# Kernel optimization log

Hardware: AMD Instinct MI355X
Metric: run time of the kernel (lower is better)

The kernel has to match this reference:

```python
import jax, jax.numpy as jnp
import numpy as np

WAY, NQ, C, H = 5, 150, 640, 10
TEMP, TEMP_ATTN = 0.2, 5.0


def _conv2d(x, w):
    return jax.lax.conv_general_dilated(x, w, (1, 1), ((0, 0), (0, 0)),
                                        dimension_numbers=('NCHW', 'OIHW', 'NCHW'))


def _conv3d(x, w, pad):
    return jax.lax.conv_general_dilated(x, w, (1, 1, 1), pad,
                                        dimension_numbers=('NCDHW', 'OIDHW', 'NCDHW'))


def _affine(x, g, b):
    # eval-mode BatchNorm folded to per-channel affine
    sh = (1, -1) + (1,) * (x.ndim - 2)
    return x * g.reshape(sh) + b.reshape(sh)


def _gnorm(x, axis, eps=1e-5):
    m = jnp.mean(x, axis=axis, keepdims=True)
    v = jnp.var(x, axis=axis, ddof=1, keepdims=True)  # torch.var is unbiased
    return (x - m) / jnp.sqrt(v + eps)


def _sep_conv4d(x, w2, g2, b2, w1, g1, b1, wp, gp, bp):
    # RENet SepConv4d: 3x3 conv over (Hs,Ws), relu, 3x3 conv over (Hq,Wq), 1x1 channel proj
    B, c, u, v, h, w = x.shape
    y = x.reshape(B, c, u, v, h * w)
    y = _conv3d(y, w2, ((1, 1), (1, 1), (0, 0)))  # kernel (3,3,1) over (u,v)
    y = jax.nn.relu(_affine(y, g2, b2))
    y = y.reshape(B, c, u * v, h, w)
    y = _conv3d(y, w1, ((0, 0), (1, 1), (1, 1)))  # kernel (1,3,3) over (h,w)
    y = _affine(y, g1, b1)
    y = _conv2d(y.reshape(B, c, u * v * h, w), wp)  # 1x1 projection to out channels
    y = _affine(y, gp, bp)
    return y.reshape(B, wp.shape[0], u, v, h, w)


def setup_inputs() -> dict:
    key = jax.random.key(0)
    ks = jax.random.split(key, 10)
    d = {}
    d['spt'] = jax.random.normal(ks[0], (1, WAY, C, H, H), jnp.float32)
    d['qry'] = jax.random.normal(ks[1], (NQ, C, H, H), jnp.float32)
    d['cca1x1_w'] = jax.random.normal(ks[2], (64, C, 1, 1), jnp.float32) * 0.05
    d['cca1x1_g'] = jnp.ones((64,), jnp.float32)
    d['cca1x1_b'] = jnp.zeros((64,), jnp.float32)
    # SepConv4d layer 0: 1 -> 16 channels
    d['s0_w2'] = jax.random.normal(ks[3], (1, 1, 3, 3, 1), jnp.float32) * 0.3
    d['s0_g2'] = jnp.ones((1,), jnp.float32); d['s0_b2'] = jnp.zeros((1,), jnp.float32)
    d['s0_w1'] = jax.random.normal(ks[4], (1, 1, 1, 3, 3), jnp.float32) * 0.3
    d['s0_g1'] = jnp.ones((1,), jnp.float32); d['s0_b1'] = jnp.zeros((1,), jnp.float32)
    d['s0_wp'] = jax.random.normal(ks[5], (16, 1, 1, 1), jnp.float32) * 0.3
    d['s0_gp'] = jnp.ones((16,), jnp.float32); d['s0_bp'] = jnp.zeros((16,), jnp.float32)
    # SepConv4d layer 1: 16 -> 1 channels
    d['s1_w2'] = jax.random.normal(ks[6], (16, 16, 3, 3, 1), jnp.float32) * 0.1
    d['s1_g2'] = jnp.ones((16,), jnp.float32); d['s1_b2'] = jnp.zeros((16,), jnp.float32)
    d['s1_w1'] = jax.random.normal(ks[7], (16, 16, 1, 3, 3), jnp.float32) * 0.1
    d['s1_g1'] = jnp.ones((16,), jnp.float32); d['s1_b1'] = jnp.zeros((16,), jnp.float32)
    d['s1_wp'] = jax.random.normal(ks[8], (1, 16, 1, 1), jnp.float32) * 0.3
    d['s1_gp'] = jnp.ones((1,), jnp.float32); d['s1_bp'] = jnp.zeros((1,), jnp.float32)
    return d


def reference(spt, qry, cca1x1_w, cca1x1_g, cca1x1_b,
              s0_w2, s0_g2, s0_b2, s0_w1, s0_g1, s0_b1, s0_wp, s0_gp, s0_bp,
              s1_w2, s1_g2, s1_b2, s1_w1, s1_g1, s1_b1, s1_wp, s1_gp, s1_bp):
    spt = spt[0]                                             # [way, C, H, W]
    spt = spt - jnp.mean(spt, axis=1, keepdims=True)         # normalize_feature
    qry = qry - jnp.mean(qry, axis=1, keepdims=True)

    def feat(x):
        y = jax.nn.relu(_affine(_conv2d(x, cca1x1_w), cca1x1_g, cca1x1_b))
        n = jnp.sqrt(jnp.sum(y * y, axis=1, keepdims=True))
        return y / jnp.maximum(n, 1e-8)                      # F.normalize(p=2, dim=1)

    s, q = feat(spt), feat(qry)                              # [way,64,H,W], [nq,64,H,W]
    corr = jnp.einsum('wcij,qckl->qwijkl', s, q)             # [nq,way,Hs,Ws,Hq,Wq]
    nq, way, Hs, Ws, Hq, Wq = corr.shape

    x = corr.reshape(nq * way, 1, Hs, Ws, Hq, Wq)
    x = _sep_conv4d(x, s0_w2, s0_g2, s0_b2, s0_w1, s0_g1, s0_b1, s0_wp, s0_gp, s0_bp)
    x = jax.nn.relu(x)
    x = _sep_conv4d(x, s1_w2, s1_g2, s1_b2, s1_w1, s1_g1, s1_b1, s1_wp, s1_gp, s1_bp)

    cs = _gnorm(x.reshape(nq, way, Hs * Ws, Hq, Wq), 2)
    cq = _gnorm(x.reshape(nq, way, Hs, Ws, Hq * Wq), 4)
    a_s = jax.nn.softmax(cs / TEMP_ATTN, axis=2).reshape(nq, way, Hs, Ws, Hq, Wq).sum(axis=(4, 5))
    a_q = jax.nn.softmax(cq / TEMP_ATTN, axis=4).reshape(nq, way, Hs, Ws, Hq, Wq).sum(axis=(2, 3))

    sp = (a_s[:, :, None] * spt[None]).mean(axis=(-1, -2))   # [nq,way,C]
    qp = (a_q[:, :, None] * qry[:, None]).mean(axis=(-1, -2))
    num = jnp.sum(sp * qp, axis=-1)
    den = jnp.maximum(jnp.linalg.norm(sp, axis=-1), 1e-8) * jnp.maximum(jnp.linalg.norm(qp, axis=-1), 1e-8)
    return (num / den) / TEMP                                # [nq, way]
```

## Files before the change

kernel.cpp:

```cpp
#include <hip/hip_runtime.h>
#include <cstdint>
#include <cstddef>

#define NQT   150
#define WAYT  5
#define CCH   640

typedef _Float16 f16;
typedef _Float16 f16x2 __attribute__((ext_vector_type(2)));
typedef _Float16 f16x4 __attribute__((ext_vector_type(4)));
typedef _Float16 f16x8 __attribute__((ext_vector_type(8)));
typedef float    f32x4 __attribute__((ext_vector_type(4)));

static __device__ __forceinline__ f16x2 pkrtz(float a, float b){
  return __builtin_bit_cast(f16x2, __builtin_amdgcn_cvt_pkrtz(a, b));
}

#define CP_A     0
#define CP_B     16
#define CP_G2    32
#define CP_B2    48
#define CP_W20   64
#define CP_W10   73
#define CP_SC    82
#define CP_T9    96
#define GS_STRIDE 1076

static __device__ __forceinline__ float stencil9(int k, int n, const float* __restrict__ w9){
  if (k >= 100 || n >= 100) return 0.f;
  const int a = n/10, b = n%10, a2 = k/10, b2 = k%10;
  const int dA = a2 - a + 1, dB = b2 - b + 1;
  if ((unsigned)dA > 2u || (unsigned)dB > 2u) return 0.f;
  return w9[dA*3 + dB];
}

__global__ __launch_bounds__(256) void k_prep_all(
    const float* __restrict__ W,
    const float* __restrict__ s0_w2, const float* __restrict__ s0_g2, const float* __restrict__ s0_b2,
    const float* __restrict__ s0_w1, const float* __restrict__ s0_g1, const float* __restrict__ s0_b1,
    const float* __restrict__ s0_wp, const float* __restrict__ s0_gp, const float* __restrict__ s0_bp,
    const float* __restrict__ s1_w2, const float* __restrict__ s1_g2, const float* __restrict__ s1_b2,
    const float* __restrict__ s1_w1, const float* __restrict__ s1_g1, const float* __restrict__ s1_b1,
    const float* __restrict__ s1_wp, const float* __restrict__ s1_gp, const float* __restrict__ s1_bp,
    float* __restrict__ cp, f16* __restrict__ Apack, f16* __restrict__ Wf2,
    f16* __restrict__ MuF, f16* __restrict__ MhF,
    f16* __restrict__ W65, float* __restrict__ wsum)
{
  const int b = blockIdx.x, t = threadIdx.x;
  if (b == 0){
    for (int e = t; e < 2560; e += 256){
      int p = e / 512, r = e % 512, l = r / 8, j = r % 8;
      int kb = l >> 4;
      int tap = 2*p + (kb >> 1);
      int cin = (kb & 1)*8 + j;
      int co = l & 15;
      float v = 0.f;
      if (tap <= 8){
        int du = tap / 3, dv = tap % 3;
        v = s1_w2[((co*16 + cin)*3 + du)*3 + dv];
      }
      Apack[e] = (f16)v;
    }
    const float gp1 = s1_gp[0];
    {
      int l = t >> 2, j = t & 3;
      int tap = l & 15, ci = ((l >> 4) << 2) + j;
      float v = 0.f;
      if (tap <= 8){
        for (int co = 0; co < 16; co++)
          v += gp1 * s1_wp[co] * s1_g1[co] * s1_w1[(co*16 + ci)*9 + tap];
      }
      Wf2[t] = (f16)v;
    }
    if (t < 144){
      int tap = t / 16, co = t % 16;
      float s = 0.f;
      for (int cin = 0; cin < 16; cin++){
        float wv = (float)(f16)s1_w2[((co*16 + cin)*3 + tap/3)*3 + tap%3];
        float rb = fmaxf((float)(f16)s0_bp[cin], 0.f);
        s += wv * rb;
      }
      cp[CP_T9 + t] = s;
    }
    if (t < 16){
      cp[CP_A + t]  = s0_gp[t] * s0_wp[t];
      cp[CP_B + t]  = s0_bp[t];
      cp[CP_G2 + t] = s1_g2[t];
      cp[CP_B2 + t] = s1_b2[t];
    }
    if (t < 9){ cp[CP_W20 + t] = s0_w2[t]; cp[CP_W10 + t] = s0_w1[t]; }
    if (t == 0){
      cp[CP_SC + 0] = s0_g2[0]; cp[CP_SC + 1] = s0_b2[0];
      cp[CP_SC + 2] = s0_g1[0]; cp[CP_SC + 3] = s0_b1[0];
      float kk = 0.f;
      for (int co = 0; co < 16; co++) kk += s1_wp[co] * s1_b1[co];
      cp[CP_SC + 4] = gp1 * kk + s1_bp[0];
    }
  } else if (b <= 14){
    const bool isMu = (b <= 7);
    f16* dst = isMu ? MuF : MhF;
    const float* w9 = isMu ? s0_w2 : s0_w1;
    const int base = (isMu ? (b-1) : (b-8)) * 2048;
    #pragma unroll
    for (int e2 = 0; e2 < 8; e2++){
      const int idx = base + e2*256 + t;
      const int j = idx & 7, l2 = (idx >> 3) & 63, ktnt = idx >> 9;
      const int kt = ktnt & 3, nt = ktnt >> 2;
      const int n = nt*16 + (l2 & 15);
      const int k = kt*32 + ((l2 >> 4) & 3)*8 + j;
      dst[idx] = (f16)stencil9(k, n, w9);
    }
  } else if (b <= 39){
    const int base = (b - 15) * 2048;
    #pragma unroll
    for (int e2 = 0; e2 < 8; e2++){
      const int idx = base + e2*256 + t;
      const int row = idx / 640, c = idx - row*640;
      float v = 0.f;
      if (row < 64) v = W[row*640 + c];
      else if (row == 64) v = 1.f;
      W65[idx] = (f16)v;
    }
  } else {
    const int o = t >> 2, qq = t & 3;
    float s = 0.f;
    for (int c = qq; c < 640; c += 4) s += W[o*640 + c];
    s += __shfl_xor(s, 1); s += __shfl_xor(s, 2);
    if (qq == 0) wsum[o] = s;
  }
}

__device__ __forceinline__ void feat_stage(const float* __restrict__ x, int kt, f16* __restrict__ dst, int t){
  for (int e = t; e < 800; e += 256){
    const int cc = e & 31, qd = e >> 5;
    const float4 v4 = ((const float4*)(x + (size_t)(kt*32 + cc)*100))[qd];
    const int pb = qd*4;
    dst[(pb+0)*40 + cc] = (f16)v4.x;
    dst[(pb+1)*40 + cc] = (f16)v4.y;
    dst[(pb+2)*40 + cc] = (f16)v4.z;
    dst[(pb+3)*40 + cc] = (f16)v4.w;
  }
}

__global__ __launch_bounds__(256) void k_feat(
    const float* __restrict__ spt, const float* __restrict__ qry,
    const f16* __restrict__ W65, const float* __restrict__ wsum,
    const float* __restrict__ gg, const float* __restrict__ bb,
    f16* __restrict__ s16, f16* __restrict__ q16,
    float* __restrict__ sptm, float* __restrict__ qrym)
{
  __shared__ f16 Xs[2][112*40];
  __shared__ float Ys[112*85];
  __shared__ float sg[64], sb[64], sw[64];
  const int n = blockIdx.x;
  const float* x; f16* out16; float* mout;
  if (n < 5){ x = spt + (size_t)n*64000; out16 = s16 + (size_t)n*7168; mout = sptm + n*100; }
  else { x = qry + (size_t)(n-5)*64000; out16 = q16 + (size_t)(n-5)*7168; mout = qrym + (size_t)(n-5)*100; }
  const int t = threadIdx.x, l = t & 63, wid = t >> 6;
  const int r16 = l & 15, kbq = (l >> 4) & 3;

  int mts[9], nts[9];
  #pragma unroll
  for (int s = 0; s < 9; s++){ const int mn = wid + s*4; mts[s] = mn/7; nts[s] = mn - (mn/7)*7; }
  f32x4 acc[9];
  #pragma unroll
  for (int s = 0; s < 9; s++) acc[s] = (f32x4){0.f,0.f,0.f,0.f};

  feat_stage(x, 0, Xs[0], t);
  __syncthreads();
  for (int kt = 0; kt < 20; kt++){
    if (kt < 19) feat_stage(x, kt+1, Xs[(kt+1)&1], t);
    const f16* xb = Xs[kt&1];
    #pragma unroll
    for (int s = 0; s < 9; s++){
      const int mn = wid + s*4;
      if (mn < 35){
        const f16x8 a8 = *(const f16x8*)(W65 + (size_t)(mts[s]*16 + r16)*640 + kt*32 + kbq*8);
        const f16x8 b8 = *(const f16x8*)(xb + (nts[s]*16 + r16)*40 + kbq*8);
        acc[s] = __builtin_amdgcn_mfma_f32_16x16x32_f16(a8, b8, acc[s], 0, 0, 0);
      }
    }
    __syncthreads();
  }
  #pragma unroll
  for (int s = 0; s < 9; s++){
    const int mn = wid + s*4;
    if (mn < 35){
      const int col = nts[s]*16 + r16, rb = mts[s]*16 + kbq*4;
      #pragma unroll
      for (int r = 0; r < 4; r++) Ys[col*85 + rb + r] = acc[s][r];
    }
  }
  if (t < 64){ sg[t] = gg[t]; sb[t] = bb[t]; sw[t] = wsum[t]; }
  __syncthreads();

  const int pix = t >> 1, half = t & 1;
  if (pix < 112){
    float yr[32]; float ssq = 0.f;
    const float m = Ys[pix*85 + 64] * (1.f/640.f);
    #pragma unroll
    for (int j = 0; j < 32; j++){
      const int o = half*32 + j;
      float yv = 0.f;
      if (pix < 100) yv = fmaxf(sg[o]*(Ys[pix*85 + o] - sw[o]*m) + sb[o], 0.f);
      yr[j] = yv; ssq += yv*yv;
    }
    ssq += __shfl_xor(ssq, 1);
    const float inv = (pix < 100) ? (1.f / fmaxf(sqrtf(ssq), 1e-8f)) : 0.f;
    #pragma unroll
    for (int j = 0; j < 16; j++){
      f16x2 hv = { (f16)(yr[2*j]*inv), (f16)(yr[2*j+1]*inv) };
      *(f16x2*)(out16 + pix*64 + half*32 + 2*j) = hv;
    }
    if (half == 0 && pix < 100) mout[pix] = m;
  }
}

__global__ __launch_bounds__(256, 3) void k_z(
    const f16* __restrict__ s16, const f16* __restrict__ q16,
    const float* __restrict__ cp, const f16* __restrict__ MuF, const f16* __restrict__ MhF,
    f16* __restrict__ z)
{
  __shared__ __align__(16) f16 smz[112*120 + 112*120 + 16];
  f16* cbT = smz;
  f16* tS  = smz + 112*120;
  const int pair = blockIdx.x;
  const int q = pair / WAYT, w = pair % WAYT;
  const int t = threadIdx.x, l = t & 63, wid = t >> 6;
  const int r16 = l & 15, kb = (l >> 4) & 3;

  {
    const f16x8 z8 = {(f16)0,(f16)0,(f16)0,(f16)0,(f16)0,(f16)0,(f16)0,(f16)0};
    if (t < 112){
      *(f16x8*)(cbT + t*120 + 112) = z8;
      *(f16x8*)(tS  + t*120 + 112) = z8;
    }
    if (t < 16) tS[112*120 + t] = (f16)0;
    if (t >= 240 && t < 248) tS[t - 240] = (f16)0;
  }

  const f16* sbase = s16 + (size_t)w * 7168;
  const f16* qbase = q16 + (size_t)q * 7168;

  for (int mn = wid; mn < 49; mn += 4){
    const int mt = mn / 7, nt = mn - (mn/7)*7;
    const f16x8 a0 = *(const f16x8*)(sbase + (mt*16 + r16)*64 + kb*8);
    const f16x8 a1 = *(const f16x8*)(sbase + (mt*16 + r16)*64 + 32 + kb*8);
    const f16x8 b0 = *(const f16x8*)(qbase + (nt*16 + r16)*64 + kb*8);
    const f16x8 b1 = *(const f16x8*)(qbase + (nt*16 + r16)*64 + 32 + kb*8);
    f32x4 acc = {0.f,0.f,0.f,0.f};
    acc = __builtin_amdgcn_mfma_f32_16x16x32_f16(a0, b0, acc, 0, 0, 0);
    acc = __builtin_amdgcn_mfma_f32_16x16x32_f16(a1, b1, acc, 0, 0, 0);
    union { f16x4 v4; f16x2 h2[2]; } hv;
    hv.h2[0] = pkrtz(acc[0], acc[1]);
    hv.h2[1] = pkrtz(acc[2], acc[3]);
    *(f16x4*)(cbT + (nt*16 + r16)*120 + mt*16 + kb*4) = hv.v4;
  }
  __syncthreads();

  const float g20 = cp[CP_SC+0], b20 = cp[CP_SC+1];
  for (int mn = wid; mn < 49; mn += 4){
    const int mt = mn / 7, nt = mn - (mn/7)*7;
    f32x4 acc = {0.f,0.f,0.f,0.f};
    #pragma unroll
    for (int kt = 0; kt < 4; kt++){
      const f16x8 a8 = *(const f16x8*)(cbT + (mt*16 + r16)*120 + kt*32 + kb*8);
      const f16x8 b8 = *(const f16x8*)(MuF + (size_t)(nt*4 + kt)*512 + l*8);
      acc = __builtin_amdgcn_mfma_f32_16x16x32_f16(a8, b8, acc, 0, 0, 0);
    }
    union { f16x4 v4; f16x2 h2[2]; } hv;
    hv.h2[0] = pkrtz(fmaxf(g20*acc[0] + b20, 0.f), fmaxf(g20*acc[1] + b20, 0.f));
    hv.h2[1] = pkrtz(fmaxf(g20*acc[2] + b20, 0.f), fmaxf(g20*acc[3] + b20, 0.f));
    *(f16x4*)(tS + (nt*16 + r16)*120 + mt*16 + kb*4) = hv.v4;
  }
  __syncthreads();

  const float g10 = cp[CP_SC+2], b10 = cp[CP_SC+3];
  for (int mn = wid; mn < 49; mn += 4){
    const int mt = mn / 7, nt = mn - (mn/7)*7;
    f32x4 acc = {0.f,0.f,0.f,0.f};
    #pragma unroll
    for (int kt = 0; kt < 4; kt++){
      const f16x8 a8 = *(const f16x8*)(tS + (mt*16 + r16)*120 + kt*32 + kb*8);
      const f16x8 b8 = *(const f16x8*)(MhF + (size_t)(nt*4 + kt)*512 + l*8);
      acc = __builtin_amdgcn_mfma_f32_16x16x32_f16(a8, b8, acc, 0, 0, 0);
    }
    const int hw = nt*16 + r16;
    if (hw < 100){
      #pragma unroll
      for (int r = 0; r < 4; r++){
        const int uv = mt*16 + kb*4 + r;
        if (uv < 100) z[(size_t)pair*10000 + uv*100 + hw] = (f16)(g10*acc[r] + b10);
      }
    }
  }
}

__global__ __launch_bounds__(256, 6) void k_l1(
    const f16* __restrict__ z, const float* __restrict__ cp,
    const f16* __restrict__ Apack, const f16* __restrict__ Wf2, f16* __restrict__ F)
{
  __shared__ f16 z3[3*1216];
  __shared__ f16 Gs[9*GS_STRIDE];
  const int u = blockIdx.x, pair = blockIdx.y;
  const int t = threadIdx.x, l = t & 63, wid = t >> 6;
  const int r16 = l & 15, kb = (l >> 4) & 3;
  const int khi = kb & 1, half = kb >> 1;

  for (int e = t; e < 1824; e += 256){
    const int du = e / 608, c2 = e - du*608;
    const int ur = u + du - 1;
    const int colb = c2*2;
    const int g = colb - 100;
    f16x2 v = {(f16)0, (f16)0};
    if (ur >= 0 && ur <= 9 && g >= 0 && g < 1000)
      v = *(const f16x2*)(z + (size_t)pair*10000 + ur*1000 + g);
    *(f16x2*)(z3 + du*1216 + colb) = v;
  }

  f16x2 Ac2[4], Bc2[4];
  {
    const float4 a4a = ((const float4*)(cp + CP_A))[khi*2];
    const float4 a4b = ((const float4*)(cp + CP_A))[khi*2+1];
    const float4 b4a = ((const float4*)(cp + CP_B))[khi*2];
    const float4 b4b = ((const float4*)(cp + CP_B))[khi*2+1];
    Ac2[0] = (f16x2){(f16)a4a.x,(f16)a4a.y}; Ac2[1] = (f16x2){(f16)a4a.z,(f16)a4a.w};
    Ac2[2] = (f16x2){(f16)a4b.x,(f16)a4b.y}; Ac2[3] = (f16x2){(f16)a4b.z,(f16)a4b.w};
    Bc2[0] = (f16x2){(f16)b4a.x,(f16)b4a.y}; Bc2[1] = (f16x2){(f16)b4a.z,(f16)b4a.w};
    Bc2[2] = (f16x2){(f16)b4b.x,(f16)b4b.y}; Bc2[3] = (f16x2){(f16)b4b.z,(f16)b4b.w};
  }
  f16x8 af[5];
  #pragma unroll
  for (int p = 0; p < 5; p++) af[p] = ((const f16x8*)Apack)[p*64 + l];
  const f16x4 wf = ((const f16x4*)Wf2)[l];

  float gv[4], bm[4], bv0[4], bv9[4];
  #pragma unroll
  for (int r = 0; r < 4; r++){
    const int co = kb*4 + r;
    gv[r] = cp[CP_G2 + co];
    const float b0 = cp[CP_B2 + co];
    float c0 = 0.f, cv0 = 0.f, cv9 = 0.f;
    #pragma unroll
    for (int du = 0; du < 3; du++){
      const int ur = u + du - 1;
      const float t0 = cp[CP_T9 + (du*3+0)*16 + co];
      const float t1 = cp[CP_T9 + (du*3+1)*16 + co];
      const float t2 = cp[CP_T9 + (du*3+2)*16 + co];
      if (ur < 0 || ur > 9) c0 += t0 + t1 + t2;
      else { cv0 += t0; cv9 += t2; }
    }
    bm[r]  = b0 - gv[r]*c0;
    bv0[r] = bm[r] - gv[r]*cv0;
    bv9[r] = bm[r] - gv[r]*cv9;
  }
  int zoffE[5];
  #pragma unroll
  for (int p = 0; p < 5; p++){
    const int tap = 2*p + half;
    const int du = (tap <= 8) ? tap/3 : 0;
    const int dv = (tap <= 8) ? tap%3 : 0;
    zoffE[p] = du*1216 + dv*100;
  }
  __syncthreads();

  const f16x2 zero2 = {(f16)0, (f16)0};
  #pragma unroll 1
  for (int i = 0; i < 16; i++){
    const int cbase = wid*256 + i*16;
    if (cbase >= 1008) break;
    const int c = cbase + r16;
    const int v = (c * 5243) >> 19;
    f32x4 acc = {0.f,0.f,0.f,0.f};
    #pragma unroll
    for (int p = 0; p < 5; p++){
      const f16 zv = z3[zoffE[p] + c];
      const f16x2 zz = {zv, zv};
      union { f16x8 v8; f16x2 h2[4]; } bu;
      #pragma unroll
      for (int j2 = 0; j2 < 4; j2++){
        f16x2 r2 = Ac2[j2] * zz + Bc2[j2];
        bu.h2[j2] = __builtin_elementwise_max(r2, zero2);
      }
      acc = __builtin_amdgcn_mfma_f32_16x16x32_f16(af[p], bu.v8, acc, 0, 0, 0);
    }
    const bool isv0 = (v == 0), isv9 = (v == 9);
    float rr[4];
    #pragma unroll
    for (int r = 0; r < 4; r++){
      const float bsel = isv0 ? bv0[r] : (isv9 ? bv9[r] : bm[r]);
      rr[r] = fmaxf(fmaf(gv[r], acc[r], bsel), 0.f);
    }
    union { f16x4 v4; f16x2 h2[2]; } t1u;
    t1u.h2[0] = pkrtz(rr[0], rr[1]);
    t1u.h2[1] = pkrtz(rr[2], rr[3]);
    f32x4 g = {0.f,0.f,0.f,0.f};
    g = __builtin_amdgcn_mfma_f32_16x16x16f16(wf, t1u.v4, g, 0, 0, 0);
    #pragma unroll
    for (int r = 0; r < 4; r++){
      const int tap = kb*4 + r;
      if (tap <= 8) Gs[tap*GS_STRIDE + 16 + c] = (f16)g[r];
    }
  }
  __syncthreads();

  const float Kc = cp[CP_SC+4];
  #pragma unroll 1
  for (int oo = 0; oo < 4; oo++){
    const int c = t + oo*256;
    if (c < 1000){
      const int hw = c - ((c * 5243) >> 19) * 100;
      const int h = (hw * 205) >> 11, w2 = hw - h*10;
      float o = Kc;
      #pragma unroll
      for (int dh = 0; dh < 3; dh++){
        #pragma unroll
        for (int dw = 0; dw < 3; dw++){
          const bool okg = ((unsigned)(h + dh - 1) <= 9u) && ((unsigned)(w2 + dw - 1) <= 9u);
          const float gvv = (float)Gs[(dh*3+dw)*GS_STRIDE + 16 + c + (dh-1)*10 + (dw-1)];
          o += okg ? gvv : 0.f;
        }
      }
      F[(size_t)pair*10000 + u*1000 + c] = (f16)o;
    }
  }
}

__global__ __launch_bounds__(256) void k_attn_a(const f16* __restrict__ F, float* __restrict__ asq)
{
  __shared__ float fb[100*101 + 4];
  __shared__ float isc[100], ccs[100], isr[100], ccr[100];
  const int pair = blockIdx.x;
  const int t = threadIdx.x;
  const float L2T = 1.4426950408889634f * 0.2f;

  for (int e = t; e < 10000; e += 256)
    fb[(e/100)*101 + (e%100)] = (float)F[(size_t)pair*10000 + e];
  __syncthreads();

  {
    const int line = t & 127;
    const bool isCol = t < 128;
    if (line < 100){
      const int base = isCol ? line : line*101;
      const int stride = isCol ? 101 : 1;
      float s = 0.f, ss = 0.f;
      for (int i = 0; i < 100; i++){ const float x = fb[base + i*stride]; s += x; ss += x*x; }
      const float m = s * 0.01f;
      const float var = (ss - 100.f*m*m) * (1.f/99.f);
      const float is2 = rsqrtf(var + 1e-5f) * L2T;
      float S = 0.f;
      for (int i = 0; i < 100; i++) S += exp2f((fb[base + i*stride] - m) * is2);
      const float cc = m*is2 + log2f(S);
      if (isCol){ isc[line] = is2; ccs[line] = cc; }
      else      { isr[line] = is2; ccr[line] = cc; }
    }
  }
  __syncthreads();
  {
    const int line = t & 127;
    if (line < 100){
      if (t < 128){
        float a = 0.f;
        for (int k = 0; k < 100; k++)
          a += exp2f(fb[line*101 + k] * isc[k] - ccs[k]);
        asq[(size_t)pair*256 + line] = a;
      } else {
        float a = 0.f;
        for (int k = 0; k < 100; k++)
          a += exp2f(fb[k*101 + line] * isr[k] - ccr[k]);
        asq[(size_t)pair*256 + 128 + line] = a;
      }
    } else {
      asq[(size_t)pair*256 + (t < 128 ? t : t)] = 0.f;
    }
  }
}

__global__ __launch_bounds__(256) void k_spqp(
    const float* __restrict__ spt, const float* __restrict__ qry,
    const float* __restrict__ asq, float* __restrict__ P)
{
  const int b = blockIdx.x;
  const int t = threadIdx.x, l = t & 63, wid = t >> 6;
  const int r16 = l & 15, kb = (l >> 4) & 3;

  if (b < 50){
    const int w = b / 10, c0 = (b % 10) * 64;
    const int c = c0 + wid*16 + r16;
    f16x8 bf[4];
    #pragma unroll
    for (int kt = 0; kt < 4; kt++){
      const int kbase = kt*32 + kb*8;
      float v[8];
      #pragma unroll
      for (int j = 0; j < 8; j++){
        const int k = kbase + j;
        v[j] = (k < 100) ? spt[(size_t)w*64000 + (size_t)c*100 + k] : 0.f;
      }
      union { f16x8 v8; f16x2 h2[4]; } u;
      #pragma unroll
      for (int j2 = 0; j2 < 4; j2++) u.h2[j2] = pkrtz(v[2*j2], v[2*j2+1]);
      bf[kt] = u.v8;
    }
    #pragma unroll 1
    for (int mt = 0; mt < 10; mt++){
      const int qr = mt*16 + r16;
      f32x4 acc = {0.f,0.f,0.f,0.f};
      #pragma unroll
      for (int kt = 0; kt < 4; kt++){
        const int kbase = kt*32 + kb*8;
        float v[8];
        #pragma unroll
        for (int j = 0; j < 8; j++)
          v[j] = (qr < 150) ? asq[(size_t)(qr*5 + w)*256 + kbase + j] : 0.f;
        union { f16x8 v8; f16x2 h2[4]; } u;
        #pragma unroll
        for (int j2 = 0; j2 < 4; j2++) u.h2[j2] = pkrtz(v[2*j2], v[2*j2+1]);
        acc = __builtin_amdgcn_mfma_f32_16x16x32_f16(u.v8, bf[kt], acc, 0, 0, 0);
      }
      #pragma unroll
      for (int r = 0; r < 4; r++){
        const int q2 = mt*16 + kb*4 + r;
        if (q2 < 150) P[(size_t)(q2*5 + w)*1280 + c0 + wid*16 + (l & 15)] = acc[r];
      }
    }
  } else {
    const int q = b - 50;
    f16x8 af[4];
    #pragma unroll
    for (int kt = 0; kt < 4; kt++){
      const int kbase = kt*32 + kb*8;
      float v[8];
      #pragma unroll
      for (int j = 0; j < 8; j++)
        v[j] = (r16 < 5) ? asq[(size_t)(q*5 + r16)*256 + 128 + kbase + j] : 0.f;
      union { f16x8 v8; f16x2 h2[4]; } u;
      #pragma unroll
      for (int j2 = 0; j2 < 4; j2++) u.h2[j2] = pkrtz(v[2*j2], v[2*j2+1]);
      af[kt] = u.v8;
    }
    #pragma unroll 1
    for (int nt = wid; nt < 40; nt += 4){
      const int c = nt*16 + r16;
      f32x4 acc = {0.f,0.f,0.f,0.f};
      #pragma unroll
      for (int kt = 0; kt < 4; kt++){
        const int kbase = kt*32 + kb*8;
        float v[8];
        #pragma unroll
        for (int j = 0; j < 8; j++){
          const int k = kbase + j;
          v[j] = (k < 100) ? qry[(size_t)q*64000 + (size_t)c*100 + k] : 0.f;
        }
        union { f16x8 v8; f16x2 h2[4]; } u;
        #pragma unroll
        for (int j2 = 0; j2 < 4; j2++) u.h2[j2] = pkrtz(v[2*j2], v[2*j2+1]);
        acc = __builtin_amdgcn_mfma_f32_16x16x32_f16(af[kt], u.v8, acc, 0, 0, 0);
      }
      #pragma unroll
      for (int r = 0; r < 4; r++){
        const int w2 = kb*4 + r;
        if (w2 < 5) P[(size_t)(q*5 + w2)*1280 + 640 + nt*16 + (l & 15)] = acc[r];
      }
    }
  }
}

__global__ __launch_bounds__(256) void k_cos(
    const float* __restrict__ P, const float* __restrict__ asq,
    const float* __restrict__ sptm, const float* __restrict__ qrym,
    float* __restrict__ out)
{
  __shared__ float pred[4];
  __shared__ float MsMq[2];
  __shared__ float red[12];
  const int pair = blockIdx.x;
  const int q = pair / WAYT, w = pair % WAYT;
  const int t = threadIdx.x, wid = t >> 6;

  float pm = 0.f;
  if (t < 100) pm = asq[(size_t)pair*256 + t] * sptm[w*100 + t];
  else if (t >= 128 && t < 228) pm = asq[(size_t)pair*256 + t] * qrym[q*100 + (t - 128)];
  #pragma unroll
  for (int m = 1; m < 64; m <<= 1) pm += __shfl_xor(pm, m);
  if ((t & 63) == 0) pred[wid] = pm;
  __syncthreads();
  if (t == 0) MsMq[0] = pred[0] + pred[1];
  if (t == 1) MsMq[1] = pred[2] + pred[3];
  __syncthreads();
  const float Ms = MsMq[0], Mq = MsMq[1];

  float d0 = 0.f, d1 = 0.f, d2 = 0.f;
  for (int c = t; c < 640; c += 256){
    const float sp = P[(size_t)pair*1280 + c] - Ms;
    const float qp = P[(size_t)pair*1280 + 640 + c] - Mq;
    d0 += sp*qp; d1 += sp*sp; d2 += qp*qp;
  }
  #pragma unroll
  for (int m = 1; m < 64; m <<= 1){
    d0 += __shfl_xor(d0, m); d1 += __shfl_xor(d1, m); d2 += __shfl_xor(d2, m);
  }
  if ((t & 63) == 0){ red[wid*3+0] = d0; red[wid*3+1] = d1; red[wid*3+2] = d2; }
  __syncthreads();
  if (t == 0){
    float e0 = 0.f, e1 = 0.f, e2 = 0.f;
    #pragma unroll
    for (int k = 0; k < 4; k++){ e0 += red[k*3]; e1 += red[k*3+1]; e2 += red[k*3+2]; }
    const float den = fmaxf(sqrtf(e1), 1e-8f) * fmaxf(sqrtf(e2), 1e-8f);
    out[pair] = (e0 / den) * 5.0f;
  }
}

extern "C" void kernel_launch(void* const* d_in, const int* in_sizes, int n_in,
                              void* d_out, int out_size, void* d_ws, size_t ws_size,
                              hipStream_t stream)
{
  (void)in_sizes; (void)n_in; (void)out_size; (void)ws_size;
  const float* spt = (const float*)d_in[0];
  const float* qry = (const float*)d_in[1];
  const float* Wc  = (const float*)d_in[2];
  const float* gc  = (const float*)d_in[3];
  const float* bc  = (const float*)d_in[4];

  float* ws    = (float*)d_ws;
  float* cp    = ws;
  float* wsum  = ws + 256;
  float* sptm  = ws + 320;
  float* qrym  = ws + 820;
  f16*  Apack  = (f16*)(ws + 15872);
  f16*  Wf2    = (f16*)(ws + 17152);
  f16*  W65    = (f16*)(ws + 17280);
  f16*  MuF    = (f16*)(ws + 42880);
  f16*  MhF    = (f16*)(ws + 50048);
  f16*  s16    = (f16*)(ws + 57216);
  f16*  q16    = (f16*)(ws + 75136);
  f16*  z      = (f16*)(ws + 612736);
  f16*  F      = (f16*)(ws + 4362736);
  float* asq   = ws + 75136;
  float* P     = ws + 612736;

  k_prep_all<<<41, 256, 0, stream>>>(
      Wc,
      (const float*)d_in[5],  (const float*)d_in[6],  (const float*)d_in[7],
      (const float*)d_in[8],  (const float*)d_in[9],  (const float*)d_in[10],
      (const float*)d_in[11], (const float*)d_in[12], (const float*)d_in[13],
      (const float*)d_in[14], (const float*)d_in[15], (const float*)d_in[16],
      (const float*)d_in[17], (const float*)d_in[18], (const float*)d_in[19],
      (const float*)d_in[20], (const float*)d_in[21], (const float*)d_in[22],
      cp, Apack, Wf2, MuF, MhF, W65, wsum);
  k_feat<<<155, 256, 0, stream>>>(spt, qry, W65, wsum, gc, bc, s16, q16, sptm, qrym);
  k_z<<<NQT*WAYT, 256, 0, stream>>>(s16, q16, cp, MuF, MhF, z);
  {
    dim3 grid(10, NQT*WAYT);
    k_l1<<<grid, 256, 0, stream>>>(z, cp, Apack, Wf2, F);
  }
  k_attn_a<<<NQT*WAYT, 256, 0, stream>>>(F, asq);
  k_spqp<<<200, 256, 0, stream>>>(spt, qry, asq, P);
  k_cos<<<NQT*WAYT, 256, 0, stream>>>(P, asq, sptm, qrym, (float*)d_out);
}
```

Baseline: 270.5 us.

## Split feature projection and query pooling across more blocks for occupancy

k_feat now launches four blocks per image, each covering 28 pixels with a 32-row padded tile, so 620 blocks run instead of 155 and each needs far less shared memory and fewer accumulators. k_spqp's query branch splits the 640 channels into two halves per query, giving 350 blocks. k_z drops its min-blocks-per-CU launch bound hint. The aim is to fill the GPU's compute units better on these small kernels, at the cost of repeated weight loads per block and some padded MFMA work.

```diff
diff --git a/kernel.cpp b/kernel.cpp
--- a/kernel.cpp
+++ b/kernel.cpp
@@ -130,15 +130,17 @@
   }
 }
 
-__device__ __forceinline__ void feat_stage(const float* __restrict__ x, int kt, f16* __restrict__ dst, int t){
-  for (int e = t; e < 800; e += 256){
-    const int cc = e & 31, qd = e >> 5;
-    const float4 v4 = ((const float4*)(x + (size_t)(kt*32 + cc)*100))[qd];
-    const int pb = qd*4;
-    dst[(pb+0)*40 + cc] = (f16)v4.x;
-    dst[(pb+1)*40 + cc] = (f16)v4.y;
-    dst[(pb+2)*40 + cc] = (f16)v4.z;
-    dst[(pb+3)*40 + cc] = (f16)v4.w;
+__device__ __forceinline__ void feat_stage4(const float* __restrict__ x, int pixoff, int kt,
+                                            f16* __restrict__ dst, int t){
+  if (t < 224){
+    const int cc = t / 7, qd = t % 7;
+    float4 v4 = make_float4(0.f, 0.f, 0.f, 0.f);
+    if (pixoff + qd*4 + 4 <= 100)
+      v4 = *(const float4*)(x + (size_t)(kt*32 + cc)*100 + pixoff + qd*4);
+    dst[(qd*4+0)*40 + cc] = (f16)v4.x;
+    dst[(qd*4+1)*40 + cc] = (f16)v4.y;
+    dst[(qd*4+2)*40 + cc] = (f16)v4.z;
+    dst[(qd*4+3)*40 + cc] = (f16)v4.w;
   }
 }
 
@@ -149,32 +151,41 @@
     f16* __restrict__ s16, f16* __restrict__ q16,
     float* __restrict__ sptm, float* __restrict__ qrym)
 {
-  __shared__ f16 Xs[2][112*40];
-  __shared__ float Ys[112*85];
+  __shared__ f16 Xs[2][32*40];
+  __shared__ float Ys[32*85];
   __shared__ float sg[64], sb[64], sw[64];
-  const int n = blockIdx.x;
+  const int b = blockIdx.x;
+  const int n = b >> 2, quarter = b & 3;
+  const int pixbase = quarter * 28;
   const float* x; f16* out16; float* mout;
   if (n < 5){ x = spt + (size_t)n*64000; out16 = s16 + (size_t)n*7168; mout = sptm + n*100; }
   else { x = qry + (size_t)(n-5)*64000; out16 = q16 + (size_t)(n-5)*7168; mout = qrym + (size_t)(n-5)*100; }
   const int t = threadIdx.x, l = t & 63, wid = t >> 6;
   const int r16 = l & 15, kbq = (l >> 4) & 3;
 
-  int mts[9], nts[9];
-  #pragma unroll
-  for (int s = 0; s < 9; s++){ const int mn = wid + s*4; mts[s] = mn/7; nts[s] = mn - (mn/7)*7; }
-  f32x4 acc[9];
-  #pragma unroll
-  for (int s = 0; s < 9; s++) acc[s] = (f32x4){0.f,0.f,0.f,0.f};
-
-  feat_stage(x, 0, Xs[0], t);
+  if (t < 40){
+    const f16x8 z8 = {(f16)0,(f16)0,(f16)0,(f16)0,(f16)0,(f16)0,(f16)0,(f16)0};
+    const int bu = t / 20, rr = (t % 20) / 5, o = t % 5;
+    *(f16x8*)(Xs[bu] + (28 + rr)*40 + o*8) = z8;
+  }
+  if (t >= 64 && t < 128){ sg[t-64] = gg[t-64]; sb[t-64] = bb[t-64]; sw[t-64] = wsum[t-64]; }
+
+  int mts[3], nts[3];
+  #pragma unroll
+  for (int s = 0; s < 3; s++){ const int mn = wid + s*4; mts[s] = mn >> 1; nts[s] = mn & 1; }
+  f32x4 acc[3];
+  #pragma unroll
+  for (int s = 0; s < 3; s++) acc[s] = (f32x4){0.f,0.f,0.f,0.f};
+
+  feat_stage4(x, pixbase, 0, Xs[0], t);
   __syncthreads();
   for (int kt = 0; kt < 20; kt++){
-    if (kt < 19) feat_stage(x, kt+1, Xs[(kt+1)&1], t);
+    if (kt < 19) feat_stage4(x, pixbase, kt+1, Xs[(kt+1)&1], t);
     const f16* xb = Xs[kt&1];
     #pragma unroll
-    for (int s = 0; s < 9; s++){
+    for (int s = 0; s < 3; s++){
       const int mn = wid + s*4;
-      if (mn < 35){
+      if (mn < 10){
         const f16x8 a8 = *(const f16x8*)(W65 + (size_t)(mts[s]*16 + r16)*640 + kt*32 + kbq*8);
         const f16x8 b8 = *(const f16x8*)(xb + (nts[s]*16 + r16)*40 + kbq*8);
         acc[s] = __builtin_amdgcn_mfma_f32_16x16x32_f16(a8, b8, acc[s], 0, 0, 0);
@@ -183,40 +194,41 @@
     __syncthreads();
   }
   #pragma unroll
-  for (int s = 0; s < 9; s++){
+  for (int s = 0; s < 3; s++){
     const int mn = wid + s*4;
-    if (mn < 35){
+    if (mn < 10){
       const int col = nts[s]*16 + r16, rb = mts[s]*16 + kbq*4;
       #pragma unroll
       for (int r = 0; r < 4; r++) Ys[col*85 + rb + r] = acc[s][r];
     }
   }
-  if (t < 64){ sg[t] = gg[t]; sb[t] = bb[t]; sw[t] = wsum[t]; }
-  __syncthreads();
-
-  const int pix = t >> 1, half = t & 1;
-  if (pix < 112){
-    float yr[32]; float ssq = 0.f;
-    const float m = Ys[pix*85 + 64] * (1.f/640.f);
-    #pragma unroll
-    for (int j = 0; j < 32; j++){
-      const int o = half*32 + j;
+  __syncthreads();
+
+  if (t < 224){
+    const int pixl = t >> 3, oo = t & 7;
+    const int pixg = pixbase + pixl;
+    const bool ok = (pixg < 100);
+    const float m = Ys[pixl*85 + 64] * (1.f/640.f);
+    float yr[8]; float ssq = 0.f;
+    #pragma unroll
+    for (int j = 0; j < 8; j++){
+      const int o = oo*8 + j;
       float yv = 0.f;
-      if (pix < 100) yv = fmaxf(sg[o]*(Ys[pix*85 + o] - sw[o]*m) + sb[o], 0.f);
+      if (ok) yv = fmaxf(sg[o]*(Ys[pixl*85 + o] - sw[o]*m) + sb[o], 0.f);
       yr[j] = yv; ssq += yv*yv;
     }
-    ssq += __shfl_xor(ssq, 1);
-    const float inv = (pix < 100) ? (1.f / fmaxf(sqrtf(ssq), 1e-8f)) : 0.f;
-    #pragma unroll
-    for (int j = 0; j < 16; j++){
-      f16x2 hv = { (f16)(yr[2*j]*inv), (f16)(yr[2*j+1]*inv) };
-      *(f16x2*)(out16 + pix*64 + half*32 + 2*j) = hv;
-    }
-    if (half == 0 && pix < 100) mout[pix] = m;
-  }
-}
-
-__global__ __launch_bounds__(256, 3) void k_z(
+    ssq += __shfl_xor(ssq, 1); ssq += __shfl_xor(ssq, 2); ssq += __shfl_xor(ssq, 4);
+    const float inv = ok ? (1.f / fmaxf(sqrtf(ssq), 1e-8f)) : 0.f;
+    #pragma unroll
+    for (int j2 = 0; j2 < 4; j2++){
+      f16x2 hv = { (f16)(yr[2*j2]*inv), (f16)(yr[2*j2+1]*inv) };
+      *(f16x2*)(out16 + (size_t)pixg*64 + oo*8 + 2*j2) = hv;
+    }
+    if (oo == 0 && ok) mout[pixg] = m;
+  }
+}
+
+__global__ __launch_bounds__(256) void k_z(
     const f16* __restrict__ s16, const f16* __restrict__ q16,
     const float* __restrict__ cp, const f16* __restrict__ MuF, const f16* __restrict__ MhF,
     f16* __restrict__ z)
@@ -472,7 +484,7 @@
         asq[(size_t)pair*256 + 128 + line] = a;
       }
     } else {
-      asq[(size_t)pair*256 + (t < 128 ? t : t)] = 0.f;
+      asq[(size_t)pair*256 + t] = 0.f;
     }
   }
 }
@@ -526,7 +538,7 @@
       }
     }
   } else {
-    const int q = b - 50;
+    const int idx = b - 50, q = idx >> 1, chalf = idx & 1;
     f16x8 af[4];
     #pragma unroll
     for (int kt = 0; kt < 4; kt++){
@@ -541,7 +553,7 @@
       af[kt] = u.v8;
     }
     #pragma unroll 1
-    for (int nt = wid; nt < 40; nt += 4){
+    for (int nt = chalf*20 + wid; nt < chalf*20 + 20; nt += 4){
       const int c = nt*16 + r16;
       f32x4 acc = {0.f,0.f,0.f,0.f};
       #pragma unroll
@@ -649,13 +661,13 @@
       (const float*)d_in[17], (const float*)d_in[18], (const float*)d_in[19],
       (const float*)d_in[20], (const float*)d_in[21], (const float*)d_in[22],
       cp, Apack, Wf2, MuF, MhF, W65, wsum);
-  k_feat<<<155, 256, 0, stream>>>(spt, qry, W65, wsum, gc, bc, s16, q16, sptm, qrym);
+  k_feat<<<620, 256, 0, stream>>>(spt, qry, W65, wsum, gc, bc, s16, q16, sptm, qrym);
   k_z<<<NQT*WAYT, 256, 0, stream>>>(s16, q16, cp, MuF, MhF, z);
   {
     dim3 grid(10, NQT*WAYT);
     k_l1<<<grid, 256, 0, stream>>>(z, cp, Apack, Wf2, F);
   }
   k_attn_a<<<NQT*WAYT, 256, 0, stream>>>(F, asq);
-  k_spqp<<<200, 256, 0, stream>>>(spt, qry, asq, P);
+  k_spqp<<<350, 256, 0, stream>>>(spt, qry, asq, P);
   k_cos<<<NQT*WAYT, 256, 0, stream>>>(P, asq, sptm, qrym, (float*)d_out);
 }
```

Measured after the change: 252.5 us. 1.07x faster.
